# Optimization experiments

Measured on AMD Instinct MI355X. Metric: run time of the kernel, lower is better.

Reference implementation:

```python
import jax, jax.numpy as jnp
import numpy as np

DIM = 1024
N_HEADS = 16
HEAD_DIM = DIM // N_HEADS
THETA = 10000.0


def rope_cos_sin(n, head_dim):
    # freqs_cis = polar(1, t * theta^(-2i/dim)) -> return cos/sin, shape [n, head_dim//2]
    inv = 1.0 / (THETA ** (jnp.arange(0, head_dim, 2, dtype=jnp.float32) / head_dim))
    ang = jnp.arange(n, dtype=jnp.float32)[:, None] * inv[None, :]
    return jnp.cos(ang), jnp.sin(ang)


def apply_rope(t, cos, sin):
    # t: [B, H, N, head_dim]; pairs are (t[..., 2i], t[..., 2i+1]) per view_as_complex
    tp = t.reshape(*t.shape[:-1], HEAD_DIM // 2, 2)
    re, im = tp[..., 0], tp[..., 1]
    ro = re * cos - im * sin
    io = re * sin + im * cos
    return jnp.stack([ro, io], axis=-1).reshape(t.shape)


def setup_inputs() -> dict:
    key = jax.random.key(0)
    ks = jax.random.split(key, 5)
    B, N = 2, 2048
    x = jax.random.normal(ks[0], (B, N, DIM), dtype=jnp.float32)
    s = 1.0 / np.sqrt(DIM)
    Wqkv = jax.random.normal(ks[1], (DIM, 3 * DIM), dtype=jnp.float32) * s
    bqkv = jnp.zeros((3 * DIM,), dtype=jnp.float32)
    Wproj = jax.random.normal(ks[2], (DIM, DIM), dtype=jnp.float32) * s
    bproj = jnp.zeros((DIM,), dtype=jnp.float32)
    return {"x": x, "Wqkv": Wqkv, "bqkv": bqkv, "Wproj": Wproj, "bproj": bproj}


def reference(x, Wqkv, bqkv, Wproj, bproj):
    B, N, C = x.shape
    scale = HEAD_DIM ** -0.5
    qkv = (x @ Wqkv + bqkv).reshape(B, N, 3, N_HEADS, HEAD_DIM)
    qkv = jnp.transpose(qkv, (2, 0, 3, 1, 4))  # [3, B, H, N, hd]
    q, k, v = qkv[0], qkv[1], qkv[2]
    cos, sin = rope_cos_sin(N, HEAD_DIM)  # [N, hd//2], broadcast over B,H
    q = apply_rope(q, cos, sin)
    k = apply_rope(k, cos, sin)
    attn = jnp.einsum('bhqd,bhkd->bhqk', q, k) * scale
    attn = jax.nn.softmax(attn, axis=-1)
    out = jnp.einsum('bhqk,bhkd->bhqd', attn, v)
    out = jnp.transpose(out, (0, 2, 1, 3)).reshape(B, N, C)
    return out @ Wproj + bproj
```

## Files before the change

kernel.cpp:

```cpp
#include <hip/hip_runtime.h>
#include <hip/hip_bf16.h>
#include <stdint.h>

#define SEQ   2048
#define BATCH 2
#define DIM   1024
#define NHEAD 16
#define HD    64
#define NT    (BATCH*SEQ)
#define N3    (3*DIM)
#define QSCALE 0.180336881f

typedef __attribute__((ext_vector_type(4)))  float f32x4;
typedef __attribute__((ext_vector_type(16))) float f32x16;
typedef __attribute__((ext_vector_type(8)))  short s16x8;
typedef __attribute__((ext_vector_type(4)))  unsigned short u16x4;
typedef __attribute__((ext_vector_type(4)))  unsigned int u32x4;

__device__ __forceinline__ unsigned short f2bf(float x){
  union { float f; uint32_t u; } v; v.f = x;
  return (unsigned short)((v.u + 0x7fffu + ((v.u >> 16) & 1u)) >> 16);
}
__device__ __forceinline__ float bf2f(unsigned short u){
  union { uint32_t u; float f; } v; v.u = ((uint32_t)u) << 16;
  return v.f;
}
__device__ __forceinline__ unsigned int cvtpk(float lo, float hi){
  unsigned int r;
  asm("v_cvt_pk_bf16_f32 %0, %1, %2" : "=v"(r) : "v"(lo), "v"(hi));
  return r;
}
__device__ __forceinline__ void gload16(const void* g, void* l){
  __builtin_amdgcn_global_load_lds((const __attribute__((address_space(1))) void*)g,
                                   (__attribute__((address_space(3))) void*)l, 16, 0, 0);
}
__device__ __forceinline__ f32x16 zero16(){
  f32x16 z;
#pragma unroll
  for (int i=0;i<16;i++) z[i]=0.f;
  return z;
}
#define MFMA(a,b,c)   __builtin_amdgcn_mfma_f32_16x16x32_bf16((a),(b),(c),0,0,0)
#define MFMA32(a,b,c) __builtin_amdgcn_mfma_f32_32x32x16_bf16((a),(b),(c),0,0,0)

__global__ __launch_bounds__(256) void k_ropetab(float2* __restrict__ cs){
  const int idx = blockIdx.x*256 + threadIdx.x;
  const int t = idx >> 5, i = idx & 31;
  const float ang = (float)t * exp2f((float)i * -0.41524101186f);
  float sn, c; sincosf(ang, &sn, &c);
  cs[idx] = make_float2(c, sn);
}

__global__ __launch_bounds__(256) void k_split(const float* __restrict__ in,
                                               unsigned short* __restrict__ hi,
                                               unsigned short* __restrict__ lo, int n4){
  int i = blockIdx.x*256 + threadIdx.x;
  if (i >= n4) return;
  f32x4 v = ((const f32x4*)in)[i];
  u16x4 h, l;
#pragma unroll
  for (int e=0;e<4;e++){ unsigned short hh = f2bf(v[e]); h[e]=hh; l[e]=f2bf(v[e]-bf2f(hh)); }
  ((u16x4*)hi)[i]=h; ((u16x4*)lo)[i]=l;
}

__global__ void k_splitT(const float* __restrict__ in,
                         unsigned short* __restrict__ hiT,
                         unsigned short* __restrict__ loT, int R, int C){
  __shared__ float t[32][33];
  int c0 = blockIdx.x*32, r0 = blockIdx.y*32;
  int tx = threadIdx.x, ty = threadIdx.y;
#pragma unroll
  for (int j=0;j<32;j+=8) t[ty+j][tx] = in[(size_t)(r0+ty+j)*C + c0+tx];
  __syncthreads();
#pragma unroll
  for (int j=0;j<32;j+=8){
    float v = t[tx][ty+j];
    unsigned short hh = f2bf(v);
    size_t o = (size_t)(c0+ty+j)*R + r0+tx;
    hiT[o]=hh; loT[o]=f2bf(v-bf2f(hh));
  }
}

__global__ void k_transT(const float* __restrict__ in,
                         unsigned short* __restrict__ oT, int R, int C){
  __shared__ float t[32][33];
  int c0 = blockIdx.x*32, r0 = blockIdx.y*32;
  int tx = threadIdx.x, ty = threadIdx.y;
#pragma unroll
  for (int j=0;j<32;j+=8) t[ty+j][tx] = in[(size_t)(r0+ty+j)*C + c0+tx];
  __syncthreads();
#pragma unroll
  for (int j=0;j<32;j+=8)
    oT[(size_t)(c0+ty+j)*R + r0+tx] = f2bf(t[tx][ty+j]);
}

__global__ __launch_bounds__(256) void k_transV(const unsigned short* __restrict__ v,
                                                unsigned short* __restrict__ vT){
  __shared__ unsigned short t[64][65];
  const int bh = blockIdx.y, t0 = blockIdx.x*64;
  const int tid = threadIdx.x;
  const size_t base = (size_t)bh*SEQ*HD;
  const int r = tid>>3, c = (tid&7)*8;
#pragma unroll
  for (int it=0; it<2; ++it){
    const int row = it*32 + r;
    s16x8 val = *(const s16x8*)(v + base + (size_t)(t0+row)*HD + c);
#pragma unroll
    for (int e=0;e<8;e++) t[row][c+e] = (unsigned short)val[e];
  }
  __syncthreads();
#pragma unroll
  for (int it=0; it<2; ++it){
    const int drow = it*32 + r;
    s16x8 o;
#pragma unroll
    for (int e=0;e<8;e++) o[e] = (short)t[c+e][drow];
    *(s16x8*)(vT + base + (size_t)drow*SEQ + t0 + c) = o;
  }
}

__global__ __launch_bounds__(256) void k_gemm(
    const unsigned short* __restrict__ Ahi, const unsigned short* __restrict__ Alo,
    const unsigned short* __restrict__ Bhi, const unsigned short* __restrict__ Blo,
    const float* __restrict__ bias, const float2* __restrict__ cstab,
    unsigned short* __restrict__ qb, unsigned short* __restrict__ kbp,
    unsigned short* __restrict__ vbp){
  __shared__ unsigned short sA[2][128*32];
  __shared__ unsigned short sB[2][128*32];
  const int tid = threadIdx.x;
  const int w = tid>>6, lane = tid&63;
  const int lr = lane&15, lk = lane>>4;
  const int wm = (w>>1)*64, wn = (w&1)*64;
  const int m0 = blockIdx.y*128, n0 = blockIdx.x*128;

  f32x4 acc[4][4];
#pragma unroll
  for (int m=0;m<4;m++)
#pragma unroll
    for (int n=0;n<4;n++) acc[m][n] = (f32x4){0.f,0.f,0.f,0.f};

  const int srow  = lane>>2;
  const int sbyte = (lane&3)*16;

  for (int kt=0; kt<1024/32; ++kt){
    const int k0 = kt*32;
#pragma unroll
    for (int cc=0; cc<2; ++cc){
      const int chunk = w*2+cc;
      const int row = chunk*16 + srow;
      const size_t aoff = ((size_t)(m0+row)*1024 + k0)*2 + sbyte;
      const size_t boff = ((size_t)(n0+row)*1024 + k0)*2 + sbyte;
      gload16((const char*)Ahi + aoff, (char*)(&sA[0][0]) + chunk*1024);
      gload16((const char*)Bhi + boff, (char*)(&sB[0][0]) + chunk*1024);
      gload16((const char*)Alo + aoff, (char*)(&sA[1][0]) + chunk*1024);
      gload16((const char*)Blo + boff, (char*)(&sB[1][0]) + chunk*1024);
    }
    __syncthreads();

    s16x8 ah[4], al[4], bh[4], bl[4];
#pragma unroll
    for (int m=0;m<4;m++){
      const int off = (wm + m*16 + lr)*64 + lk*16;
      ah[m] = *(const s16x8*)((const char*)(&sA[0][0]) + off);
      al[m] = *(const s16x8*)((const char*)(&sA[1][0]) + off);
    }
#pragma unroll
    for (int n=0;n<4;n++){
      const int off = (wn + n*16 + lr)*64 + lk*16;
      bh[n] = *(const s16x8*)((const char*)(&sB[0][0]) + off);
      bl[n] = *(const s16x8*)((const char*)(&sB[1][0]) + off);
    }
#pragma unroll
    for (int m=0;m<4;m++)
#pragma unroll
      for (int n=0;n<4;n++){
        acc[m][n] = MFMA(ah[m], bh[n], acc[m][n]);
        acc[m][n] = MFMA(ah[m], bl[n], acc[m][n]);
        acc[m][n] = MFMA(al[m], bh[n], acc[m][n]);
      }
    __syncthreads();
  }

#pragma unroll
  for (int m=0;m<4;m++)
#pragma unroll
    for (int n=0;n<4;n++)
#pragma unroll
      for (int r=0;r<4;r++){
        const int gm = m0 + wm + m*16 + lk*4 + r;
        const int gn = n0 + wn + n*16 + lr;
        float val = acc[m][n][r] + bias[gn];
        const int three = gn>>10, rem = gn&1023, h = rem>>6, d = rem&63;
        const int b = gm>>11, t = gm&2047;
        const float partner = __shfl_xor(val, 1);
        const size_t dst = ((size_t)(b*NHEAD + h))*SEQ*HD + (size_t)t*HD + d;
        if (three < 2){
          const float2 cs = cstab[t*32 + (d>>1)];
          float o;
          if (d & 1) o = partner*cs.y + val*cs.x;
          else       o = val*cs.x - partner*cs.y;
          if (three==0) qb[dst] = f2bf(o*QSCALE);
          else          kbp[dst] = f2bf(o);
        } else {
          vbp[dst] = f2bf(val);
        }
      }
}

__global__ __launch_bounds__(256) void k_gemmP(
    const unsigned short* __restrict__ A, const unsigned short* __restrict__ B,
    const float* __restrict__ bias, float* __restrict__ outp){
  __shared__ unsigned short sA[128*32];
  __shared__ unsigned short sB[64*32];
  const int tid = threadIdx.x;
  const int w = tid>>6, lane = tid&63;
  const int lr = lane&15, lk = lane>>4;
  const int m0 = blockIdx.y*128, n0 = blockIdx.x*64;

  f32x4 acc[2][4];
#pragma unroll
  for (int m=0;m<2;m++)
#pragma unroll
    for (int n=0;n<4;n++) acc[m][n] = (f32x4){0.f,0.f,0.f,0.f};

  const int srow  = lane>>2;
  const int sbyte = (lane&3)*16;

  for (int kt=0; kt<1024/32; ++kt){
    const int k0 = kt*32;
#pragma unroll
    for (int cc=0; cc<2; ++cc){
      const int chunk = w*2+cc;
      const int row = chunk*16 + srow;
      gload16((const char*)A + ((size_t)(m0+row)*1024 + k0)*2 + sbyte,
              (char*)sA + chunk*1024);
    }
    {
      const int row = w*16 + srow;
      gload16((const char*)B + ((size_t)(n0+row)*1024 + k0)*2 + sbyte,
              (char*)sB + w*1024);
    }
    __syncthreads();

    s16x8 ah[2], bh[4];
#pragma unroll
    for (int m=0;m<2;m++)
      ah[m] = *(const s16x8*)((const char*)sA + (w*32 + m*16 + lr)*64 + lk*16);
#pragma unroll
    for (int n=0;n<4;n++)
      bh[n] = *(const s16x8*)((const char*)sB + (n*16 + lr)*64 + lk*16);
#pragma unroll
    for (int m=0;m<2;m++)
#pragma unroll
      for (int n=0;n<4;n++)
        acc[m][n] = MFMA(ah[m], bh[n], acc[m][n]);
    __syncthreads();
  }

#pragma unroll
  for (int m=0;m<2;m++)
#pragma unroll
    for (int n=0;n<4;n++)
#pragma unroll
      for (int r=0;r<4;r++){
        const int gm = m0 + w*32 + m*16 + lk*4 + r;
        const int gn = n0 + n*16 + lr;
        outp[(size_t)gm*DIM + gn] = acc[m][n][r] + bias[gn];
      }
}

__global__ __launch_bounds__(256) void k_attn(const unsigned short* __restrict__ qb,
                                              const unsigned short* __restrict__ kb,
                                              const unsigned short* __restrict__ vTb,
                                              unsigned short* __restrict__ ao){
  __shared__ float l_tab[4][32];
  const int flat = blockIdx.x;
  const int wi = (flat & 7)*64 + (flat >> 3);
  const int bh = wi >> 4, qt = wi & 15;
  const int wid = threadIdx.x >> 6, lane = threadIdx.x & 63;
  const int col = lane & 31, hi = lane >> 5;
  const size_t base = (size_t)bh*SEQ*HD;
  const int q0 = qt*128 + wid*32;

  s16x8 qf[4];
  {
    const unsigned short* qp = qb + base + (size_t)(q0+col)*HD + hi*8;
#pragma unroll
    for (int hb=0;hb<4;hb++) qf[hb] = *(const s16x8*)(qp + hb*16);
  }

  f32x16 o0 = zero16(), o1 = zero16();
  float m = -INFINITY, l = 0.f;

  for (int kv0 = 0; kv0 < SEQ; kv0 += 64){
    s16x8 kf0[4], kf1[4];
    {
      const unsigned short* kp0 = kb + base + (size_t)(kv0+col)*HD + hi*8;
      const unsigned short* kp1 = kp0 + 32*HD;
#pragma unroll
      for (int hb=0;hb<4;hb++){
        kf0[hb] = *(const s16x8*)(kp0 + hb*16);
        kf1[hb] = *(const s16x8*)(kp1 + hb*16);
      }
    }
    f32x16 a0 = zero16(), a1 = zero16();
    __builtin_amdgcn_s_setprio(1);
#pragma unroll
    for (int hb=0;hb<4;hb++){
      a0 = MFMA32(kf0[hb], qf[hb], a0);
      a1 = MFMA32(kf1[hb], qf[hb], a1);
    }
    __builtin_amdgcn_s_setprio(0);

    s16x8 vf0[4], vf1[4];
    {
      const unsigned short* vp0 = vTb + base + (size_t)col*SEQ + kv0 + hi*8;
      const unsigned short* vp1 = vp0 + (size_t)32*SEQ;
#pragma unroll
      for (int mk=0;mk<4;mk++){
        vf0[mk] = *(const s16x8*)(vp0 + mk*16);
        vf1[mk] = *(const s16x8*)(vp1 + mk*16);
      }
    }

    float pm = a0[0];
#pragma unroll
    for (int i=1;i<16;i++) pm = fmaxf(pm, a0[i]);
#pragma unroll
    for (int i=0;i<16;i++) pm = fmaxf(pm, a1[i]);
    pm = fmaxf(pm, __shfl_xor(pm, 32));

    if (!__all(pm - m <= 8.0f)){
      const float mn = fmaxf(m, pm);
      const float al = __builtin_amdgcn_exp2f(m - mn);
      l *= al;
#pragma unroll
      for (int i=0;i<16;i++){ o0[i] *= al; o1[i] *= al; }
      m = mn;
    }
#pragma unroll
    for (int i=0;i<16;i++){
      a0[i] = __builtin_amdgcn_exp2f(a0[i] - m);
      a1[i] = __builtin_amdgcn_exp2f(a1[i] - m);
    }
    float rs = 0.f;
#pragma unroll
    for (int i=0;i<16;i++) rs += a0[i] + a1[i];
    rs += __shfl_xor(rs, 32);
    l += rs;

    unsigned int pfd[4][4];
#pragma unroll
    for (int kb=0;kb<4;kb++){
      float cc[8];
#pragma unroll
      for (int j=0;j<8;j++) cc[j] = (kb<2) ? a0[(kb&1)*8+j] : a1[(kb&1)*8+j];
      unsigned int lo0 = cvtpk(cc[0],cc[1]), lo1 = cvtpk(cc[2],cc[3]);
      unsigned int h0  = cvtpk(cc[4],cc[5]), h1  = cvtpk(cc[6],cc[7]);
      unsigned int sl0 = (unsigned int)__shfl_xor((int)lo0, 32);
      unsigned int sl1 = (unsigned int)__shfl_xor((int)lo1, 32);
      unsigned int sh0 = (unsigned int)__shfl_xor((int)h0, 32);
      unsigned int sh1 = (unsigned int)__shfl_xor((int)h1, 32);
      pfd[kb][0] = hi ? sh0 : lo0;
      pfd[kb][1] = hi ? sh1 : lo1;
      pfd[kb][2] = hi ? h0  : sl0;
      pfd[kb][3] = hi ? h1  : sl1;
    }

    __builtin_amdgcn_s_setprio(1);
#pragma unroll
    for (int mk=0;mk<4;mk++){
      u32x4 dd = {pfd[mk][0], pfd[mk][1], pfd[mk][2], pfd[mk][3]};
      s16x8 pa = __builtin_bit_cast(s16x8, dd);
      o0 = MFMA32(pa, vf0[mk], o0);
      o1 = MFMA32(pa, vf1[mk], o1);
    }
    __builtin_amdgcn_s_setprio(0);
  }

  l_tab[wid][col] = 1.0f / l;
  const int b = bh >> 4, h = bh & 15;
#pragma unroll
  for (int r=0;r<16;r++){
    const int qloc = (r&3) + 8*(r>>2) + 4*hi;
    const float linv = l_tab[wid][qloc];
    const int tq = q0 + qloc;
    const size_t drow = ((size_t)(b*SEQ + tq))*DIM + h*HD + col;
    ao[drow]      = f2bf(o0[r] * linv);
    ao[drow + 32] = f2bf(o1[r] * linv);
  }
}

extern "C" void kernel_launch(void* const* d_in, const int* in_sizes, int n_in,
                              void* d_out, int out_size, void* d_ws, size_t ws_size,
                              hipStream_t stream){
  const float* x     = (const float*)d_in[0];
  const float* Wqkv  = (const float*)d_in[1];
  const float* bqkv  = (const float*)d_in[2];
  const float* Wproj = (const float*)d_in[3];
  const float* bproj = (const float*)d_in[4];
  float* out = (float*)d_out;

  char* ws = (char*)d_ws;
  size_t off = 0;
  auto alloc = [&](size_t bytes)->char*{
    char* p = ws + off; off += (bytes + 255) & ~(size_t)255; return p;
  };
  unsigned short* xhi    = (unsigned short*)alloc((size_t)NT*DIM*2);
  unsigned short* xlo    = (unsigned short*)alloc((size_t)NT*DIM*2);
  unsigned short* wqT_hi = (unsigned short*)alloc((size_t)N3*DIM*2);
  unsigned short* wqT_lo = (unsigned short*)alloc((size_t)N3*DIM*2);
  unsigned short* wpT    = (unsigned short*)alloc((size_t)DIM*DIM*2);
  unsigned short* q_bf   = (unsigned short*)alloc((size_t)NT*DIM*2);
  unsigned short* k_bf   = (unsigned short*)alloc((size_t)NT*DIM*2);
  unsigned short* v_bf   = (unsigned short*)alloc((size_t)NT*DIM*2);
  unsigned short* vT_bf  = (unsigned short*)alloc((size_t)NT*DIM*2);
  unsigned short* ao_bf  = (unsigned short*)alloc((size_t)NT*DIM*2);
  float2*         cstab  = (float2*)alloc((size_t)SEQ*32*sizeof(float2));

  k_ropetab<<<SEQ*32/256, 256, 0, stream>>>(cstab);
  k_split<<<(NT*DIM/4)/256, 256, 0, stream>>>(x, xhi, xlo, NT*DIM/4);
  k_splitT<<<dim3(N3/32, DIM/32), dim3(32,8), 0, stream>>>(Wqkv, wqT_hi, wqT_lo, DIM, N3);
  k_transT<<<dim3(DIM/32, DIM/32), dim3(32,8), 0, stream>>>(Wproj, wpT, DIM, DIM);
  k_gemm<<<dim3(N3/128, NT/128), 256, 0, stream>>>(xhi, xlo, wqT_hi, wqT_lo, bqkv, cstab,
                                                   q_bf, k_bf, v_bf);
  k_transV<<<dim3(SEQ/64, BATCH*NHEAD), 256, 0, stream>>>(v_bf, vT_bf);
  k_attn<<<dim3(512), 256, 0, stream>>>(q_bf, k_bf, vT_bf, ao_bf);
  k_gemmP<<<dim3(DIM/64, NT/128), 256, 0, stream>>>(ao_bf, wpT, bproj, out);
}
```

Baseline: 344.6 us.

## Drop split-bf16 QKV GEMM and software-pipeline K/V loads in attention

```diff
diff --git a/kernel.cpp b/kernel.cpp
--- a/kernel.cpp
+++ b/kernel.cpp
@@ -21,10 +21,6 @@
   union { float f; uint32_t u; } v; v.f = x;
   return (unsigned short)((v.u + 0x7fffu + ((v.u >> 16) & 1u)) >> 16);
 }
-__device__ __forceinline__ float bf2f(unsigned short u){
-  union { uint32_t u; float f; } v; v.u = ((uint32_t)u) << 16;
-  return v.f;
-}
 __device__ __forceinline__ unsigned int cvtpk(float lo, float hi){
   unsigned int r;
   asm("v_cvt_pk_bf16_f32 %0, %1, %2" : "=v"(r) : "v"(lo), "v"(hi));
@@ -51,34 +47,15 @@
   cs[idx] = make_float2(c, sn);
 }
 
-__global__ __launch_bounds__(256) void k_split(const float* __restrict__ in,
-                                               unsigned short* __restrict__ hi,
-                                               unsigned short* __restrict__ lo, int n4){
+__global__ __launch_bounds__(256) void k_tobf(const float* __restrict__ in,
+                                              unsigned short* __restrict__ o, int n4){
   int i = blockIdx.x*256 + threadIdx.x;
   if (i >= n4) return;
   f32x4 v = ((const f32x4*)in)[i];
-  u16x4 h, l;
-#pragma unroll
-  for (int e=0;e<4;e++){ unsigned short hh = f2bf(v[e]); h[e]=hh; l[e]=f2bf(v[e]-bf2f(hh)); }
-  ((u16x4*)hi)[i]=h; ((u16x4*)lo)[i]=l;
-}
-
-__global__ void k_splitT(const float* __restrict__ in,
-                         unsigned short* __restrict__ hiT,
-                         unsigned short* __restrict__ loT, int R, int C){
-  __shared__ float t[32][33];
-  int c0 = blockIdx.x*32, r0 = blockIdx.y*32;
-  int tx = threadIdx.x, ty = threadIdx.y;
-#pragma unroll
-  for (int j=0;j<32;j+=8) t[ty+j][tx] = in[(size_t)(r0+ty+j)*C + c0+tx];
-  __syncthreads();
-#pragma unroll
-  for (int j=0;j<32;j+=8){
-    float v = t[tx][ty+j];
-    unsigned short hh = f2bf(v);
-    size_t o = (size_t)(c0+ty+j)*R + r0+tx;
-    hiT[o]=hh; loT[o]=f2bf(v-bf2f(hh));
-  }
+  u16x4 h;
+#pragma unroll
+  for (int e=0;e<4;e++) h[e] = f2bf(v[e]);
+  ((u16x4*)o)[i] = h;
 }
 
 __global__ void k_transT(const float* __restrict__ in,
@@ -120,13 +97,12 @@
 }
 
 __global__ __launch_bounds__(256) void k_gemm(
-    const unsigned short* __restrict__ Ahi, const unsigned short* __restrict__ Alo,
-    const unsigned short* __restrict__ Bhi, const unsigned short* __restrict__ Blo,
+    const unsigned short* __restrict__ A, const unsigned short* __restrict__ B,
     const float* __restrict__ bias, const float2* __restrict__ cstab,
     unsigned short* __restrict__ qb, unsigned short* __restrict__ kbp,
     unsigned short* __restrict__ vbp){
-  __shared__ unsigned short sA[2][128*32];
-  __shared__ unsigned short sB[2][128*32];
+  __shared__ unsigned short sA[128*32];
+  __shared__ unsigned short sB[128*32];
   const int tid = threadIdx.x;
   const int w = tid>>6, lane = tid&63;
   const int lr = lane&15, lk = lane>>4;
@@ -148,36 +124,23 @@
     for (int cc=0; cc<2; ++cc){
       const int chunk = w*2+cc;
       const int row = chunk*16 + srow;
-      const size_t aoff = ((size_t)(m0+row)*1024 + k0)*2 + sbyte;
-      const size_t boff = ((size_t)(n0+row)*1024 + k0)*2 + sbyte;
-      gload16((const char*)Ahi + aoff, (char*)(&sA[0][0]) + chunk*1024);
-      gload16((const char*)Bhi + boff, (char*)(&sB[0][0]) + chunk*1024);
-      gload16((const char*)Alo + aoff, (char*)(&sA[1][0]) + chunk*1024);
-      gload16((const char*)Blo + boff, (char*)(&sB[1][0]) + chunk*1024);
+      gload16((const char*)A + ((size_t)(m0+row)*1024 + k0)*2 + sbyte, (char*)sA + chunk*1024);
+      gload16((const char*)B + ((size_t)(n0+row)*1024 + k0)*2 + sbyte, (char*)sB + chunk*1024);
     }
     __syncthreads();
 
-    s16x8 ah[4], al[4], bh[4], bl[4];
-#pragma unroll
-    for (int m=0;m<4;m++){
-      const int off = (wm + m*16 + lr)*64 + lk*16;
-      ah[m] = *(const s16x8*)((const char*)(&sA[0][0]) + off);
-      al[m] = *(const s16x8*)((const char*)(&sA[1][0]) + off);
-    }
-#pragma unroll
-    for (int n=0;n<4;n++){
-      const int off = (wn + n*16 + lr)*64 + lk*16;
-      bh[n] = *(const s16x8*)((const char*)(&sB[0][0]) + off);
-      bl[n] = *(const s16x8*)((const char*)(&sB[1][0]) + off);
-    }
+    s16x8 ah[4], bh[4];
 #pragma unroll
     for (int m=0;m<4;m++)
-#pragma unroll
-      for (int n=0;n<4;n++){
+      ah[m] = *(const s16x8*)((const char*)sA + (wm + m*16 + lr)*64 + lk*16);
+#pragma unroll
+    for (int n=0;n<4;n++)
+      bh[n] = *(const s16x8*)((const char*)sB + (wn + n*16 + lr)*64 + lk*16);
+#pragma unroll
+    for (int m=0;m<4;m++)
+#pragma unroll
+      for (int n=0;n<4;n++)
         acc[m][n] = MFMA(ah[m], bh[n], acc[m][n]);
-        acc[m][n] = MFMA(ah[m], bl[n], acc[m][n]);
-        acc[m][n] = MFMA(al[m], bh[n], acc[m][n]);
-      }
     __syncthreads();
   }
 
@@ -269,10 +232,83 @@
       }
 }
 
-__global__ __launch_bounds__(256) void k_attn(const unsigned short* __restrict__ qb,
-                                              const unsigned short* __restrict__ kb,
-                                              const unsigned short* __restrict__ vTb,
-                                              unsigned short* __restrict__ ao){
+#define LOADK(kv, K0, K1) { \
+  const unsigned short* kp_ = kbase + (size_t)((kv)+col)*HD + hi*8; \
+  _Pragma("unroll") \
+  for (int hb=0; hb<4; hb++){ \
+    K0[hb] = *(const s16x8*)(kp_ + hb*16); \
+    K1[hb] = *(const s16x8*)(kp_ + 32*HD + hb*16); } }
+
+#define LOADV(kv, V0, V1) { \
+  const unsigned short* vp_ = vbase + (size_t)col*SEQ + (kv) + hi*8; \
+  _Pragma("unroll") \
+  for (int mk=0; mk<4; mk++){ \
+    V0[mk] = *(const s16x8*)(vp_ + mk*16); \
+    V1[mk] = *(const s16x8*)(vp_ + (size_t)32*SEQ + mk*16); } }
+
+#define TILE(K0c, K1c, V0c, V1c, kvn, K0n, K1n, V0n, V1n) { \
+  f32x16 a0 = zero16(), a1 = zero16(); \
+  __builtin_amdgcn_s_setprio(1); \
+  _Pragma("unroll") \
+  for (int hb=0; hb<4; hb++){ \
+    a0 = MFMA32(K0c[hb], qf[hb], a0); \
+    a1 = MFMA32(K1c[hb], qf[hb], a1); } \
+  __builtin_amdgcn_s_setprio(0); \
+  LOADK(kvn, K0n, K1n); \
+  LOADV(kvn, V0n, V1n); \
+  float pm0 = fmaxf(a0[0], a0[1]), pm1 = fmaxf(a0[2], a0[3]); \
+  _Pragma("unroll") \
+  for (int i=4;i<16;i+=2){ pm0 = fmaxf(pm0, a0[i]); pm1 = fmaxf(pm1, a0[i+1]); } \
+  _Pragma("unroll") \
+  for (int i=0;i<16;i+=2){ pm0 = fmaxf(pm0, a1[i]); pm1 = fmaxf(pm1, a1[i+1]); } \
+  float pm = fmaxf(pm0, pm1); \
+  pm = fmaxf(pm, __shfl_xor(pm, 32)); \
+  if (!__all(pm - m <= 8.0f)){ \
+    const float mn = fmaxf(m, pm); \
+    const float al = __builtin_amdgcn_exp2f(m - mn); \
+    l *= al; \
+    _Pragma("unroll") \
+    for (int i=0;i<16;i++){ o0[i] *= al; o1[i] *= al; } \
+    m = mn; \
+  } \
+  _Pragma("unroll") \
+  for (int i=0;i<16;i++){ \
+    a0[i] = __builtin_amdgcn_exp2f(a0[i] - m); \
+    a1[i] = __builtin_amdgcn_exp2f(a1[i] - m); } \
+  float rs = 0.f; \
+  _Pragma("unroll") \
+  for (int i=0;i<16;i++) rs += a0[i] + a1[i]; \
+  rs += __shfl_xor(rs, 32); \
+  l += rs; \
+  unsigned int pfd[4][4]; \
+  _Pragma("unroll") \
+  for (int kb2=0; kb2<4; kb2++){ \
+    float cc[8]; \
+    _Pragma("unroll") \
+    for (int j=0;j<8;j++) cc[j] = (kb2<2) ? a0[(kb2&1)*8+j] : a1[(kb2&1)*8+j]; \
+    unsigned int lo0 = cvtpk(cc[0],cc[1]), lo1 = cvtpk(cc[2],cc[3]); \
+    unsigned int h0  = cvtpk(cc[4],cc[5]), h1  = cvtpk(cc[6],cc[7]); \
+    unsigned int sl0 = (unsigned int)__shfl_xor((int)lo0, 32); \
+    unsigned int sl1 = (unsigned int)__shfl_xor((int)lo1, 32); \
+    unsigned int sh0 = (unsigned int)__shfl_xor((int)h0, 32); \
+    unsigned int sh1 = (unsigned int)__shfl_xor((int)h1, 32); \
+    pfd[kb2][0] = hi ? sh0 : lo0; \
+    pfd[kb2][1] = hi ? sh1 : lo1; \
+    pfd[kb2][2] = hi ? h0  : sl0; \
+    pfd[kb2][3] = hi ? h1  : sl1; } \
+  __builtin_amdgcn_s_setprio(1); \
+  _Pragma("unroll") \
+  for (int mk=0; mk<4; mk++){ \
+    u32x4 dd = {pfd[mk][0], pfd[mk][1], pfd[mk][2], pfd[mk][3]}; \
+    s16x8 pa = __builtin_bit_cast(s16x8, dd); \
+    o0 = MFMA32(pa, V0c[mk], o0); \
+    o1 = MFMA32(pa, V1c[mk], o1); } \
+  __builtin_amdgcn_s_setprio(0); }
+
+__global__ __launch_bounds__(256, 2) void k_attn(const unsigned short* __restrict__ qb,
+                                                 const unsigned short* __restrict__ kb,
+                                                 const unsigned short* __restrict__ vTb,
+                                                 unsigned short* __restrict__ ao){
   __shared__ float l_tab[4][32];
   const int flat = blockIdx.x;
   const int wi = (flat & 7)*64 + (flat >> 3);
@@ -281,6 +317,8 @@
   const int col = lane & 31, hi = lane >> 5;
   const size_t base = (size_t)bh*SEQ*HD;
   const int q0 = qt*128 + wid*32;
+  const unsigned short* kbase = kb + base;
+  const unsigned short* vbase = vTb + base;
 
   s16x8 qf[4];
   {
@@ -292,90 +330,15 @@
   f32x16 o0 = zero16(), o1 = zero16();
   float m = -INFINITY, l = 0.f;
 
-  for (int kv0 = 0; kv0 < SEQ; kv0 += 64){
-    s16x8 kf0[4], kf1[4];
-    {
-      const unsigned short* kp0 = kb + base + (size_t)(kv0+col)*HD + hi*8;
-      const unsigned short* kp1 = kp0 + 32*HD;
-#pragma unroll
-      for (int hb=0;hb<4;hb++){
-        kf0[hb] = *(const s16x8*)(kp0 + hb*16);
-        kf1[hb] = *(const s16x8*)(kp1 + hb*16);
-      }
-    }
-    f32x16 a0 = zero16(), a1 = zero16();
-    __builtin_amdgcn_s_setprio(1);
-#pragma unroll
-    for (int hb=0;hb<4;hb++){
-      a0 = MFMA32(kf0[hb], qf[hb], a0);
-      a1 = MFMA32(kf1[hb], qf[hb], a1);
-    }
-    __builtin_amdgcn_s_setprio(0);
-
-    s16x8 vf0[4], vf1[4];
-    {
-      const unsigned short* vp0 = vTb + base + (size_t)col*SEQ + kv0 + hi*8;
-      const unsigned short* vp1 = vp0 + (size_t)32*SEQ;
-#pragma unroll
-      for (int mk=0;mk<4;mk++){
-        vf0[mk] = *(const s16x8*)(vp0 + mk*16);
-        vf1[mk] = *(const s16x8*)(vp1 + mk*16);
-      }
-    }
-
-    float pm = a0[0];
-#pragma unroll
-    for (int i=1;i<16;i++) pm = fmaxf(pm, a0[i]);
-#pragma unroll
-    for (int i=0;i<16;i++) pm = fmaxf(pm, a1[i]);
-    pm = fmaxf(pm, __shfl_xor(pm, 32));
-
-    if (!__all(pm - m <= 8.0f)){
-      const float mn = fmaxf(m, pm);
-      const float al = __builtin_amdgcn_exp2f(m - mn);
-      l *= al;
-#pragma unroll
-      for (int i=0;i<16;i++){ o0[i] *= al; o1[i] *= al; }
-      m = mn;
-    }
-#pragma unroll
-    for (int i=0;i<16;i++){
-      a0[i] = __builtin_amdgcn_exp2f(a0[i] - m);
-      a1[i] = __builtin_amdgcn_exp2f(a1[i] - m);
-    }
-    float rs = 0.f;
-#pragma unroll
-    for (int i=0;i<16;i++) rs += a0[i] + a1[i];
-    rs += __shfl_xor(rs, 32);
-    l += rs;
-
-    unsigned int pfd[4][4];
-#pragma unroll
-    for (int kb=0;kb<4;kb++){
-      float cc[8];
-#pragma unroll
-      for (int j=0;j<8;j++) cc[j] = (kb<2) ? a0[(kb&1)*8+j] : a1[(kb&1)*8+j];
-      unsigned int lo0 = cvtpk(cc[0],cc[1]), lo1 = cvtpk(cc[2],cc[3]);
-      unsigned int h0  = cvtpk(cc[4],cc[5]), h1  = cvtpk(cc[6],cc[7]);
-      unsigned int sl0 = (unsigned int)__shfl_xor((int)lo0, 32);
-      unsigned int sl1 = (unsigned int)__shfl_xor((int)lo1, 32);
-      unsigned int sh0 = (unsigned int)__shfl_xor((int)h0, 32);
-      unsigned int sh1 = (unsigned int)__shfl_xor((int)h1, 32);
-      pfd[kb][0] = hi ? sh0 : lo0;
-      pfd[kb][1] = hi ? sh1 : lo1;
-      pfd[kb][2] = hi ? h0  : sl0;
-      pfd[kb][3] = hi ? h1  : sl1;
-    }
-
-    __builtin_amdgcn_s_setprio(1);
-#pragma unroll
-    for (int mk=0;mk<4;mk++){
-      u32x4 dd = {pfd[mk][0], pfd[mk][1], pfd[mk][2], pfd[mk][3]};
-      s16x8 pa = __builtin_bit_cast(s16x8, dd);
-      o0 = MFMA32(pa, vf0[mk], o0);
-      o1 = MFMA32(pa, vf1[mk], o1);
-    }
-    __builtin_amdgcn_s_setprio(0);
+  s16x8 kf0A[4], kf1A[4], vf0A[4], vf1A[4];
+  s16x8 kf0B[4], kf1B[4], vf0B[4], vf1B[4];
+
+  LOADK(0, kf0A, kf1A);
+  LOADV(0, vf0A, vf1A);
+
+  for (int kv0 = 0; kv0 < SEQ; kv0 += 128){
+    TILE(kf0A, kf1A, vf0A, vf1A, kv0+64, kf0B, kf1B, vf0B, vf1B);
+    TILE(kf0B, kf1B, vf0B, vf1B, (kv0+128)&(SEQ-1), kf0A, kf1A, vf0A, vf1A);
   }
 
   l_tab[wid][col] = 1.0f / l;
@@ -406,24 +369,21 @@
   auto alloc = [&](size_t bytes)->char*{
     char* p = ws + off; off += (bytes + 255) & ~(size_t)255; return p;
   };
-  unsigned short* xhi    = (unsigned short*)alloc((size_t)NT*DIM*2);
-  unsigned short* xlo    = (unsigned short*)alloc((size_t)NT*DIM*2);
-  unsigned short* wqT_hi = (unsigned short*)alloc((size_t)N3*DIM*2);
-  unsigned short* wqT_lo = (unsigned short*)alloc((size_t)N3*DIM*2);
-  unsigned short* wpT    = (unsigned short*)alloc((size_t)DIM*DIM*2);
-  unsigned short* q_bf   = (unsigned short*)alloc((size_t)NT*DIM*2);
-  unsigned short* k_bf   = (unsigned short*)alloc((size_t)NT*DIM*2);
-  unsigned short* v_bf   = (unsigned short*)alloc((size_t)NT*DIM*2);
-  unsigned short* vT_bf  = (unsigned short*)alloc((size_t)NT*DIM*2);
-  unsigned short* ao_bf  = (unsigned short*)alloc((size_t)NT*DIM*2);
-  float2*         cstab  = (float2*)alloc((size_t)SEQ*32*sizeof(float2));
+  unsigned short* xb    = (unsigned short*)alloc((size_t)NT*DIM*2);
+  unsigned short* wqT   = (unsigned short*)alloc((size_t)N3*DIM*2);
+  unsigned short* wpT   = (unsigned short*)alloc((size_t)DIM*DIM*2);
+  unsigned short* q_bf  = (unsigned short*)alloc((size_t)NT*DIM*2);
+  unsigned short* k_bf  = (unsigned short*)alloc((size_t)NT*DIM*2);
+  unsigned short* v_bf  = (unsigned short*)alloc((size_t)NT*DIM*2);
+  unsigned short* vT_bf = (unsigned short*)alloc((size_t)NT*DIM*2);
+  unsigned short* ao_bf = (unsigned short*)alloc((size_t)NT*DIM*2);
+  float2*         cstab = (float2*)alloc((size_t)SEQ*32*sizeof(float2));
 
   k_ropetab<<<SEQ*32/256, 256, 0, stream>>>(cstab);
-  k_split<<<(NT*DIM/4)/256, 256, 0, stream>>>(x, xhi, xlo, NT*DIM/4);
-  k_splitT<<<dim3(N3/32, DIM/32), dim3(32,8), 0, stream>>>(Wqkv, wqT_hi, wqT_lo, DIM, N3);
+  k_tobf<<<(NT*DIM/4)/256, 256, 0, stream>>>(x, xb, NT*DIM/4);
+  k_transT<<<dim3(N3/32, DIM/32), dim3(32,8), 0, stream>>>(Wqkv, wqT, DIM, N3);
   k_transT<<<dim3(DIM/32, DIM/32), dim3(32,8), 0, stream>>>(Wproj, wpT, DIM, DIM);
-  k_gemm<<<dim3(N3/128, NT/128), 256, 0, stream>>>(xhi, xlo, wqT_hi, wqT_lo, bqkv, cstab,
-                                                   q_bf, k_bf, v_bf);
+  k_gemm<<<dim3(N3/128, NT/128), 256, 0, stream>>>(xb, wqT, bqkv, cstab, q_bf, k_bf, v_bf);
   k_transV<<<dim3(SEQ/64, BATCH*NHEAD), 256, 0, stream>>>(v_bf, vT_bf);
   k_attn<<<dim3(512), 256, 0, stream>>>(q_bf, k_bf, vT_bf, ao_bf);
   k_gemmP<<<dim3(DIM/64, NT/128), 256, 0, stream>>>(ao_bf, wpT, bproj, out);
```

Measured after the change: 277.9 us. 1.24x faster.

## Drop split-bf16 QKV GEMM and split attention KV range across two blocks

Applied to the files above, without the earlier changes.

```diff
diff --git a/kernel.cpp b/kernel.cpp
--- a/kernel.cpp
+++ b/kernel.cpp
@@ -21,10 +21,6 @@
   union { float f; uint32_t u; } v; v.f = x;
   return (unsigned short)((v.u + 0x7fffu + ((v.u >> 16) & 1u)) >> 16);
 }
-__device__ __forceinline__ float bf2f(unsigned short u){
-  union { uint32_t u; float f; } v; v.u = ((uint32_t)u) << 16;
-  return v.f;
-}
 __device__ __forceinline__ unsigned int cvtpk(float lo, float hi){
   unsigned int r;
   asm("v_cvt_pk_bf16_f32 %0, %1, %2" : "=v"(r) : "v"(lo), "v"(hi));
@@ -51,34 +47,15 @@
   cs[idx] = make_float2(c, sn);
 }
 
-__global__ __launch_bounds__(256) void k_split(const float* __restrict__ in,
-                                               unsigned short* __restrict__ hi,
-                                               unsigned short* __restrict__ lo, int n4){
+__global__ __launch_bounds__(256) void k_tobf(const float* __restrict__ in,
+                                              unsigned short* __restrict__ o, int n4){
   int i = blockIdx.x*256 + threadIdx.x;
   if (i >= n4) return;
   f32x4 v = ((const f32x4*)in)[i];
-  u16x4 h, l;
-#pragma unroll
-  for (int e=0;e<4;e++){ unsigned short hh = f2bf(v[e]); h[e]=hh; l[e]=f2bf(v[e]-bf2f(hh)); }
-  ((u16x4*)hi)[i]=h; ((u16x4*)lo)[i]=l;
-}
-
-__global__ void k_splitT(const float* __restrict__ in,
-                         unsigned short* __restrict__ hiT,
-                         unsigned short* __restrict__ loT, int R, int C){
-  __shared__ float t[32][33];
-  int c0 = blockIdx.x*32, r0 = blockIdx.y*32;
-  int tx = threadIdx.x, ty = threadIdx.y;
-#pragma unroll
-  for (int j=0;j<32;j+=8) t[ty+j][tx] = in[(size_t)(r0+ty+j)*C + c0+tx];
-  __syncthreads();
-#pragma unroll
-  for (int j=0;j<32;j+=8){
-    float v = t[tx][ty+j];
-    unsigned short hh = f2bf(v);
-    size_t o = (size_t)(c0+ty+j)*R + r0+tx;
-    hiT[o]=hh; loT[o]=f2bf(v-bf2f(hh));
-  }
+  u16x4 h;
+#pragma unroll
+  for (int e=0;e<4;e++) h[e] = f2bf(v[e]);
+  ((u16x4*)o)[i] = h;
 }
 
 __global__ void k_transT(const float* __restrict__ in,
@@ -120,13 +97,12 @@
 }
 
 __global__ __launch_bounds__(256) void k_gemm(
-    const unsigned short* __restrict__ Ahi, const unsigned short* __restrict__ Alo,
-    const unsigned short* __restrict__ Bhi, const unsigned short* __restrict__ Blo,
+    const unsigned short* __restrict__ A, const unsigned short* __restrict__ B,
     const float* __restrict__ bias, const float2* __restrict__ cstab,
     unsigned short* __restrict__ qb, unsigned short* __restrict__ kbp,
     unsigned short* __restrict__ vbp){
-  __shared__ unsigned short sA[2][128*32];
-  __shared__ unsigned short sB[2][128*32];
+  __shared__ unsigned short sA[128*32];
+  __shared__ unsigned short sB[128*32];
   const int tid = threadIdx.x;
   const int w = tid>>6, lane = tid&63;
   const int lr = lane&15, lk = lane>>4;
@@ -148,36 +124,23 @@
     for (int cc=0; cc<2; ++cc){
       const int chunk = w*2+cc;
       const int row = chunk*16 + srow;
-      const size_t aoff = ((size_t)(m0+row)*1024 + k0)*2 + sbyte;
-      const size_t boff = ((size_t)(n0+row)*1024 + k0)*2 + sbyte;
-      gload16((const char*)Ahi + aoff, (char*)(&sA[0][0]) + chunk*1024);
-      gload16((const char*)Bhi + boff, (char*)(&sB[0][0]) + chunk*1024);
-      gload16((const char*)Alo + aoff, (char*)(&sA[1][0]) + chunk*1024);
-      gload16((const char*)Blo + boff, (char*)(&sB[1][0]) + chunk*1024);
+      gload16((const char*)A + ((size_t)(m0+row)*1024 + k0)*2 + sbyte, (char*)sA + chunk*1024);
+      gload16((const char*)B + ((size_t)(n0+row)*1024 + k0)*2 + sbyte, (char*)sB + chunk*1024);
     }
     __syncthreads();
 
-    s16x8 ah[4], al[4], bh[4], bl[4];
-#pragma unroll
-    for (int m=0;m<4;m++){
-      const int off = (wm + m*16 + lr)*64 + lk*16;
-      ah[m] = *(const s16x8*)((const char*)(&sA[0][0]) + off);
-      al[m] = *(const s16x8*)((const char*)(&sA[1][0]) + off);
-    }
-#pragma unroll
-    for (int n=0;n<4;n++){
-      const int off = (wn + n*16 + lr)*64 + lk*16;
-      bh[n] = *(const s16x8*)((const char*)(&sB[0][0]) + off);
-      bl[n] = *(const s16x8*)((const char*)(&sB[1][0]) + off);
-    }
+    s16x8 ah[4], bh[4];
 #pragma unroll
     for (int m=0;m<4;m++)
-#pragma unroll
-      for (int n=0;n<4;n++){
+      ah[m] = *(const s16x8*)((const char*)sA + (wm + m*16 + lr)*64 + lk*16);
+#pragma unroll
+    for (int n=0;n<4;n++)
+      bh[n] = *(const s16x8*)((const char*)sB + (wn + n*16 + lr)*64 + lk*16);
+#pragma unroll
+    for (int m=0;m<4;m++)
+#pragma unroll
+      for (int n=0;n<4;n++)
         acc[m][n] = MFMA(ah[m], bh[n], acc[m][n]);
-        acc[m][n] = MFMA(ah[m], bl[n], acc[m][n]);
-        acc[m][n] = MFMA(al[m], bh[n], acc[m][n]);
-      }
     __syncthreads();
   }
 
@@ -269,18 +232,21 @@
       }
 }
 
-__global__ __launch_bounds__(256) void k_attn(const unsigned short* __restrict__ qb,
-                                              const unsigned short* __restrict__ kb,
-                                              const unsigned short* __restrict__ vTb,
-                                              unsigned short* __restrict__ ao){
-  __shared__ float l_tab[4][32];
+__global__ __launch_bounds__(256, 4) void k_attn(const unsigned short* __restrict__ qb,
+                                                 const unsigned short* __restrict__ kb,
+                                                 const unsigned short* __restrict__ vTb,
+                                                 float* __restrict__ po,
+                                                 float2* __restrict__ ml){
   const int flat = blockIdx.x;
-  const int wi = (flat & 7)*64 + (flat >> 3);
-  const int bh = wi >> 4, qt = wi & 15;
+  const int work = (flat & 7)*128 + (flat >> 3);
+  const int bhqt = work >> 1, half = work & 1;
+  const int bh = bhqt >> 4, qt = bhqt & 15;
   const int wid = threadIdx.x >> 6, lane = threadIdx.x & 63;
   const int col = lane & 31, hi = lane >> 5;
   const size_t base = (size_t)bh*SEQ*HD;
   const int q0 = qt*128 + wid*32;
+  const unsigned short* kbase = kb + base;
+  const unsigned short* vbase = vTb + base;
 
   s16x8 qf[4];
   {
@@ -292,15 +258,15 @@
   f32x16 o0 = zero16(), o1 = zero16();
   float m = -INFINITY, l = 0.f;
 
-  for (int kv0 = 0; kv0 < SEQ; kv0 += 64){
+  const int kvbeg = half*1024;
+  for (int kv0 = kvbeg; kv0 < kvbeg+1024; kv0 += 64){
     s16x8 kf0[4], kf1[4];
     {
-      const unsigned short* kp0 = kb + base + (size_t)(kv0+col)*HD + hi*8;
-      const unsigned short* kp1 = kp0 + 32*HD;
+      const unsigned short* kp = kbase + (size_t)(kv0+col)*HD + hi*8;
 #pragma unroll
       for (int hb=0;hb<4;hb++){
-        kf0[hb] = *(const s16x8*)(kp0 + hb*16);
-        kf1[hb] = *(const s16x8*)(kp1 + hb*16);
+        kf0[hb] = *(const s16x8*)(kp + hb*16);
+        kf1[hb] = *(const s16x8*)(kp + 32*HD + hb*16);
       }
     }
     f32x16 a0 = zero16(), a1 = zero16();
@@ -314,20 +280,20 @@
 
     s16x8 vf0[4], vf1[4];
     {
-      const unsigned short* vp0 = vTb + base + (size_t)col*SEQ + kv0 + hi*8;
-      const unsigned short* vp1 = vp0 + (size_t)32*SEQ;
+      const unsigned short* vp = vbase + (size_t)col*SEQ + kv0 + hi*8;
 #pragma unroll
       for (int mk=0;mk<4;mk++){
-        vf0[mk] = *(const s16x8*)(vp0 + mk*16);
-        vf1[mk] = *(const s16x8*)(vp1 + mk*16);
+        vf0[mk] = *(const s16x8*)(vp + mk*16);
+        vf1[mk] = *(const s16x8*)(vp + (size_t)32*SEQ + mk*16);
       }
     }
 
-    float pm = a0[0];
-#pragma unroll
-    for (int i=1;i<16;i++) pm = fmaxf(pm, a0[i]);
-#pragma unroll
-    for (int i=0;i<16;i++) pm = fmaxf(pm, a1[i]);
+    float pm0 = fmaxf(a0[0], a0[1]), pm1 = fmaxf(a0[2], a0[3]);
+#pragma unroll
+    for (int i=4;i<16;i+=2){ pm0 = fmaxf(pm0, a0[i]); pm1 = fmaxf(pm1, a0[i+1]); }
+#pragma unroll
+    for (int i=0;i<16;i+=2){ pm0 = fmaxf(pm0, a1[i]); pm1 = fmaxf(pm1, a1[i+1]); }
+    float pm = fmaxf(pm0, pm1);
     pm = fmaxf(pm, __shfl_xor(pm, 32));
 
     if (!__all(pm - m <= 8.0f)){
@@ -351,20 +317,20 @@
 
     unsigned int pfd[4][4];
 #pragma unroll
-    for (int kb=0;kb<4;kb++){
+    for (int kb2=0; kb2<4; kb2++){
       float cc[8];
 #pragma unroll
-      for (int j=0;j<8;j++) cc[j] = (kb<2) ? a0[(kb&1)*8+j] : a1[(kb&1)*8+j];
+      for (int j=0;j<8;j++) cc[j] = (kb2<2) ? a0[(kb2&1)*8+j] : a1[(kb2&1)*8+j];
       unsigned int lo0 = cvtpk(cc[0],cc[1]), lo1 = cvtpk(cc[2],cc[3]);
       unsigned int h0  = cvtpk(cc[4],cc[5]), h1  = cvtpk(cc[6],cc[7]);
       unsigned int sl0 = (unsigned int)__shfl_xor((int)lo0, 32);
       unsigned int sl1 = (unsigned int)__shfl_xor((int)lo1, 32);
       unsigned int sh0 = (unsigned int)__shfl_xor((int)h0, 32);
       unsigned int sh1 = (unsigned int)__shfl_xor((int)h1, 32);
-      pfd[kb][0] = hi ? sh0 : lo0;
-      pfd[kb][1] = hi ? sh1 : lo1;
-      pfd[kb][2] = hi ? h0  : sl0;
-      pfd[kb][3] = hi ? h1  : sl1;
+      pfd[kb2][0] = hi ? sh0 : lo0;
+      pfd[kb2][1] = hi ? sh1 : lo1;
+      pfd[kb2][2] = hi ? h0  : sl0;
+      pfd[kb2][3] = hi ? h1  : sl1;
     }
 
     __builtin_amdgcn_s_setprio(1);
@@ -378,17 +344,39 @@
     __builtin_amdgcn_s_setprio(0);
   }
 
-  l_tab[wid][col] = 1.0f / l;
-  const int b = bh >> 4, h = bh & 15;
 #pragma unroll
   for (int r=0;r<16;r++){
     const int qloc = (r&3) + 8*(r>>2) + 4*hi;
-    const float linv = l_tab[wid][qloc];
-    const int tq = q0 + qloc;
-    const size_t drow = ((size_t)(b*SEQ + tq))*DIM + h*HD + col;
-    ao[drow]      = f2bf(o0[r] * linv);
-    ao[drow + 32] = f2bf(o1[r] * linv);
-  }
+    const size_t orow = ((size_t)work*128 + wid*32 + qloc)*64;
+    po[orow + col]      = o0[r];
+    po[orow + 32 + col] = o1[r];
+  }
+  if (hi == 0)
+    ml[(size_t)work*128 + wid*32 + col] = make_float2(m, l);
+}
+
+__global__ __launch_bounds__(256) void k_comb(const float* __restrict__ po,
+                                              const float2* __restrict__ ml,
+                                              unsigned short* __restrict__ ao){
+  const int idx = blockIdx.x*256 + threadIdx.x;
+  const int row = idx >> 4;
+  const int dc  = (idx & 15) * 4;
+  const int bhqt = row >> 7, qrow = row & 127;
+  const float2 ml0 = ml[(size_t)(bhqt*2+0)*128 + qrow];
+  const float2 ml1 = ml[(size_t)(bhqt*2+1)*128 + qrow];
+  const float M = fmaxf(ml0.x, ml1.x);
+  const float w0 = __builtin_amdgcn_exp2f(ml0.x - M);
+  const float w1 = __builtin_amdgcn_exp2f(ml1.x - M);
+  const float inv = 1.0f / (ml0.y*w0 + ml1.y*w1);
+  const f32x4 a = *(const f32x4*)(po + ((size_t)(bhqt*2+0)*128 + qrow)*64 + dc);
+  const f32x4 b4 = *(const f32x4*)(po + ((size_t)(bhqt*2+1)*128 + qrow)*64 + dc);
+  const int bh = bhqt >> 4, qt = bhqt & 15;
+  const int b = bh >> 4, h = bh & 15;
+  const int tq = qt*128 + qrow;
+  u16x4 r;
+#pragma unroll
+  for (int e=0;e<4;e++) r[e] = f2bf((a[e]*w0 + b4[e]*w1) * inv);
+  *(u16x4*)(ao + ((size_t)(b*SEQ + tq))*DIM + h*HD + dc) = r;
 }
 
 extern "C" void kernel_launch(void* const* d_in, const int* in_sizes, int n_in,
@@ -406,25 +394,25 @@
   auto alloc = [&](size_t bytes)->char*{
     char* p = ws + off; off += (bytes + 255) & ~(size_t)255; return p;
   };
-  unsigned short* xhi    = (unsigned short*)alloc((size_t)NT*DIM*2);
-  unsigned short* xlo    = (unsigned short*)alloc((size_t)NT*DIM*2);
-  unsigned short* wqT_hi = (unsigned short*)alloc((size_t)N3*DIM*2);
-  unsigned short* wqT_lo = (unsigned short*)alloc((size_t)N3*DIM*2);
-  unsigned short* wpT    = (unsigned short*)alloc((size_t)DIM*DIM*2);
-  unsigned short* q_bf   = (unsigned short*)alloc((size_t)NT*DIM*2);
-  unsigned short* k_bf   = (unsigned short*)alloc((size_t)NT*DIM*2);
-  unsigned short* v_bf   = (unsigned short*)alloc((size_t)NT*DIM*2);
-  unsigned short* vT_bf  = (unsigned short*)alloc((size_t)NT*DIM*2);
-  unsigned short* ao_bf  = (unsigned short*)alloc((size_t)NT*DIM*2);
-  float2*         cstab  = (float2*)alloc((size_t)SEQ*32*sizeof(float2));
+  unsigned short* xb    = (unsigned short*)alloc((size_t)NT*DIM*2);
+  unsigned short* wqT   = (unsigned short*)alloc((size_t)N3*DIM*2);
+  unsigned short* wpT   = (unsigned short*)alloc((size_t)DIM*DIM*2);
+  unsigned short* q_bf  = (unsigned short*)alloc((size_t)NT*DIM*2);
+  unsigned short* k_bf  = (unsigned short*)alloc((size_t)NT*DIM*2);
+  unsigned short* v_bf  = (unsigned short*)alloc((size_t)NT*DIM*2);
+  unsigned short* vT_bf = (unsigned short*)alloc((size_t)NT*DIM*2);
+  unsigned short* ao_bf = (unsigned short*)alloc((size_t)NT*DIM*2);
+  float*          po    = (float*)alloc((size_t)1024*128*64*sizeof(float));
+  float2*         mlb   = (float2*)alloc((size_t)1024*128*sizeof(float2));
+  float2*         cstab = (float2*)alloc((size_t)SEQ*32*sizeof(float2));
 
   k_ropetab<<<SEQ*32/256, 256, 0, stream>>>(cstab);
-  k_split<<<(NT*DIM/4)/256, 256, 0, stream>>>(x, xhi, xlo, NT*DIM/4);
-  k_splitT<<<dim3(N3/32, DIM/32), dim3(32,8), 0, stream>>>(Wqkv, wqT_hi, wqT_lo, DIM, N3);
+  k_tobf<<<(NT*DIM/4)/256, 256, 0, stream>>>(x, xb, NT*DIM/4);
+  k_transT<<<dim3(N3/32, DIM/32), dim3(32,8), 0, stream>>>(Wqkv, wqT, DIM, N3);
   k_transT<<<dim3(DIM/32, DIM/32), dim3(32,8), 0, stream>>>(Wproj, wpT, DIM, DIM);
-  k_gemm<<<dim3(N3/128, NT/128), 256, 0, stream>>>(xhi, xlo, wqT_hi, wqT_lo, bqkv, cstab,
-                                                   q_bf, k_bf, v_bf);
+  k_gemm<<<dim3(N3/128, NT/128), 256, 0, stream>>>(xb, wqT, bqkv, cstab, q_bf, k_bf, v_bf);
   k_transV<<<dim3(SEQ/64, BATCH*NHEAD), 256, 0, stream>>>(v_bf, vT_bf);
-  k_attn<<<dim3(512), 256, 0, stream>>>(q_bf, k_bf, vT_bf, ao_bf);
+  k_attn<<<dim3(1024), 256, 0, stream>>>(q_bf, k_bf, vT_bf, po, mlb);
+  k_comb<<<(65536*16)/256, 256, 0, stream>>>(po, mlb, ao_bf);
   k_gemmP<<<dim3(DIM/64, NT/128), 256, 0, stream>>>(ao_bf, wpT, bproj, out);
 }
```

After: 301.0 us. 1.14x faster.
